# Performance work log

Hardware: AMD Instinct MI355X
Metric: run time of the kernel (lower is better)

The kernel has to match this reference:

```python
import jax, jax.numpy as jnp
import numpy as np

L = 4  # positional-encoding frequencies

def setup_inputs() -> dict:
    key = jax.random.key(0)
    ks = jax.random.split(key, 7)
    H, Wd, Ns = 512, 512, 8
    N = H * Wd * Ns
    f16 = jnp.float16
    return {
        "coords": jax.random.normal(ks[0], (N, 3), dtype=f16),
        "W1": (jax.random.normal(ks[1], (27, 64), dtype=jnp.float32) * 0.2).astype(f16),
        "b1": (jax.random.normal(ks[2], (64,), dtype=jnp.float32) * 0.02).astype(f16),
        "W2": (jax.random.normal(ks[3], (64, 64), dtype=jnp.float32) * 0.12).astype(f16),
        "b2": (jax.random.normal(ks[4], (64,), dtype=jnp.float32) * 0.02).astype(f16),
        "W3": (jax.random.normal(ks[5], (64, 4), dtype=jnp.float32) * 0.12).astype(f16),
        "b3": (jax.random.normal(ks[6], (4,), dtype=jnp.float32) * 0.02).astype(f16),
        "H": H,
        "W": Wd,
    }

def _positional_encoding(x):
    n = x.shape[0]
    freqs = (2.0 ** jnp.arange(L, dtype=jnp.float32)).astype(x.dtype)  # (L,)
    xf = x[:, None, :] * freqs[None, :, None]                          # (N, L, 3)
    sc = jnp.stack([jnp.sin(xf), jnp.cos(xf)], axis=2)                 # (N, L, 2, 3)
    return jnp.concatenate([x, sc.reshape(n, 2 * 3 * L)], axis=-1)

def _mlp(enc, W1, b1, W2, b2, W3, b3):
    h = jax.nn.relu(enc @ W1 + b1)
    h = jax.nn.relu(h @ W2 + b2)
    return h @ W3 + b3

def reference(coords, W1, b1, W2, b2, W3, b3, H, W):
    # The Python tile loop gathers idx_tile, runs PE+MLP, and scatters back to the
    # same idx_tile; the tiles partition [0, H*W*N_samples) exactly once, so the
    # whole forward equals a single fused PE+MLP over all coords.
    x = coords.astype(jnp.float16)
    enc = _positional_encoding(x)
    out = _mlp(enc, W1, b1, W2, b2, W3, b3)
    return out.astype(jnp.float16)  # (H*W*N_samples, 4)
```

## Files before the change

kernel.cpp:

```cpp
#include <hip/hip_runtime.h>

typedef _Float16 f16x2 __attribute__((ext_vector_type(2)));
typedef _Float16 f16x8 __attribute__((ext_vector_type(8)));
typedef float    floatx4 __attribute__((ext_vector_type(4)));
typedef unsigned uintx4 __attribute__((ext_vector_type(4)));

#define INV2PI 0.15915494309189535f
#define NP 4

__device__ __forceinline__ unsigned cvt_pk_u(float a, float b) {
    return __builtin_bit_cast(unsigned, __builtin_amdgcn_cvt_pkrtz(a, b));
}
__device__ __forceinline__ unsigned pk_relu_u(unsigned hu) {
    f16x2 h = __builtin_bit_cast(f16x2, hu);
    f16x2 z; z[0] = (_Float16)0.f; z[1] = (_Float16)0.f;
    return __builtin_bit_cast(unsigned, __builtin_elementwise_max(h, z));
}

__global__ __launch_bounds__(256, 4) void nerf_fused_kernel(
    const float* __restrict__ coords,
    const float* __restrict__ W1, const float* __restrict__ b1,
    const float* __restrict__ W2, const float* __restrict__ b2,
    const float* __restrict__ W3, const float* __restrict__ b3,
    float* __restrict__ out, int npts)
{
    __shared__ __align__(16) floatx4 wlds[14][64];

    const int tid  = threadIdx.x;
    const int wave = tid >> 6;
    const int lane = tid & 63;
    const int m    = lane & 15;
    const int g    = lane >> 4;

    if (wave == 0) {
        #pragma unroll
        for (int t1 = 0; t1 < 4; ++t1) {
            int n = t1 * 16 + m;
            f16x8 v;
            #pragma unroll
            for (int i = 0; i < 8; ++i) {
                float w;
                if (i < 6)        w = W1[(3 + 6 * g + (i >= 3 ? 3 : 0) + (i % 3)) * 64 + n];
                else if (g == 0)  w = (i == 6) ? W1[0 * 64 + n] : W1[1 * 64 + n];
                else if (g == 1)  w = (i == 6) ? W1[2 * 64 + n] : b1[n];
                else              w = 0.f;
                v[i] = (_Float16)w;
            }
            wlds[t1][lane] = __builtin_bit_cast(floatx4, v);
        }
        #pragma unroll
        for (int kk = 0; kk < 2; ++kk) {
            f16x8 v;
            #pragma unroll
            for (int i = 0; i < 8; ++i) {
                int f = ((i >> 2) + 2 * kk) * 16 + g * 4 + (i & 3);
                v[i] = (_Float16)((m < 4) ? W3[f * 4 + m] : 0.f);
            }
            wlds[12 + kk][lane] = __builtin_bit_cast(floatx4, v);
        }
    } else if (wave == 1) {
        #pragma unroll
        for (int t2 = 0; t2 < 4; ++t2) {
            int n = t2 * 16 + m;
            #pragma unroll
            for (int kk = 0; kk < 2; ++kk) {
                f16x8 v;
                #pragma unroll
                for (int i = 0; i < 8; ++i) {
                    int f = ((i >> 2) + 2 * kk) * 16 + g * 4 + (i & 3);
                    v[i] = (_Float16)W2[f * 64 + n];
                }
                wlds[4 + t2 * 2 + kk][lane] = __builtin_bit_cast(floatx4, v);
            }
        }
    }
    __syncthreads();

    floatx4 bias2q[4];
    #pragma unroll
    for (int t2 = 0; t2 < 4; ++t2)
        #pragma unroll
        for (int r = 0; r < 4; ++r)
            bias2q[t2][r] = b2[t2 * 16 + g * 4 + r];
    floatx4 bias3q;
    #pragma unroll
    for (int r = 0; r < 4; ++r)
        bias3q[r] = (g == 0) ? b3[r] : 0.f;
    const floatx4 zero4 = (floatx4){0.f, 0.f, 0.f, 0.f};

    const float sg = __builtin_amdgcn_ldexpf(INV2PI, g);

    const int  ntile = npts >> 6;
    const int  gw    = blockIdx.x * 4 + wave;
    const int  nw    = gridDim.x * 4;
    const int  niter = ntile / nw;

    const char* cptr = (const char*)coords + ((long)(gw << 6) + m) * 12;
    char*       optr = (char*)out + ((long)(gw << 6) + m) * 16;
    const long  cstride = (long)nw * 64 * 12;
    const long  ostride = (long)nw * 64 * 16;

    float cx[NP][3];
    #pragma unroll
    for (int p = 0; p < NP; ++p)
        #pragma unroll
        for (int j = 0; j < 3; ++j)
            cx[p][j] = *(const float*)(cptr + p * 192 + j * 4);
    cptr += cstride;

    for (int it = 0; it < niter; ++it) {
        unsigned fr0 = 0;
        asm volatile("" : "+v"(fr0));
        const floatx4* wp = &wlds[0][0] + fr0 + lane;

        f16x8 B1[NP];
        #pragma unroll
        for (int p = 0; p < NP; ++p) {
            float s[6];
            #pragma unroll
            for (int i = 0; i < 6; ++i) {
                float xv = cx[p][i % 3];
                float ph = (i >= 3) ? 0.25f : 0.f;
                s[i] = __builtin_amdgcn_sinf(fmaf(xv, sg, ph));
            }
            float v6 = (g == 0) ? cx[p][0] : ((g == 1) ? cx[p][2] : 0.f);
            float v7 = (g == 0) ? cx[p][1] : ((g == 1) ? 1.f : 0.f);
            uintx4 b1u;
            b1u[0] = cvt_pk_u(s[0], s[1]);
            b1u[1] = cvt_pk_u(s[2], s[3]);
            b1u[2] = cvt_pk_u(s[4], s[5]);
            b1u[3] = cvt_pk_u(v6, v7);
            B1[p] = __builtin_bit_cast(f16x8, b1u);
        }

        if (it + 1 < niter) {
            #pragma unroll
            for (int p = 0; p < NP; ++p)
                #pragma unroll
                for (int j = 0; j < 3; ++j)
                    cx[p][j] = *(const float*)(cptr + p * 192 + j * 4);
            cptr += cstride;
        }

        f16x8 B2[NP][2];
        #pragma unroll
        for (int kk = 0; kk < 2; ++kk) {
            uintx4 b2u[NP];
            #pragma unroll
            for (int tt = 0; tt < 2; ++tt) {
                f16x8 A1v = __builtin_bit_cast(f16x8, wp[(2 * kk + tt) * 64]);
                #pragma unroll
                for (int p = 0; p < NP; ++p) {
                    floatx4 a = __builtin_amdgcn_mfma_f32_16x16x32_f16(A1v, B1[p], zero4, 0, 0, 0);
                    b2u[p][2 * tt + 0] = pk_relu_u(cvt_pk_u(a[0], a[1]));
                    b2u[p][2 * tt + 1] = pk_relu_u(cvt_pk_u(a[2], a[3]));
                }
            }
            #pragma unroll
            for (int p = 0; p < NP; ++p)
                B2[p][kk] = __builtin_bit_cast(f16x8, b2u[p]);
        }

        f16x8 B3[NP][2];
        #pragma unroll
        for (int kk = 0; kk < 2; ++kk) {
            uintx4 b3u[NP];
            #pragma unroll
            for (int tt = 0; tt < 2; ++tt) {
                int t2 = 2 * kk + tt;
                f16x8 A2v0 = __builtin_bit_cast(f16x8, wp[(4 + t2 * 2) * 64]);
                f16x8 A2v1 = __builtin_bit_cast(f16x8, wp[(5 + t2 * 2) * 64]);
                #pragma unroll
                for (int p = 0; p < NP; ++p) {
                    floatx4 a = __builtin_amdgcn_mfma_f32_16x16x32_f16(A2v0, B2[p][0], bias2q[t2], 0, 0, 0);
                    a = __builtin_amdgcn_mfma_f32_16x16x32_f16(A2v1, B2[p][1], a, 0, 0, 0);
                    b3u[p][2 * tt + 0] = pk_relu_u(cvt_pk_u(a[0], a[1]));
                    b3u[p][2 * tt + 1] = pk_relu_u(cvt_pk_u(a[2], a[3]));
                }
            }
            #pragma unroll
            for (int p = 0; p < NP; ++p)
                B3[p][kk] = __builtin_bit_cast(f16x8, b3u[p]);
        }

        f16x8 A3v0 = __builtin_bit_cast(f16x8, wp[12 * 64]);
        f16x8 A3v1 = __builtin_bit_cast(f16x8, wp[13 * 64]);
        #pragma unroll
        for (int p = 0; p < NP; ++p) {
            floatx4 acc3 = __builtin_amdgcn_mfma_f32_16x16x32_f16(A3v0, B3[p][0], bias3q, 0, 0, 0);
            acc3 = __builtin_amdgcn_mfma_f32_16x16x32_f16(A3v1, B3[p][1], acc3, 0, 0, 0);
            if (g == 0)
                *(floatx4*)(optr + p * 256) = acc3;
        }
        optr += ostride;
    }
}

extern "C" void kernel_launch(void* const* d_in, const int* in_sizes, int n_in,
                              void* d_out, int out_size, void* d_ws, size_t ws_size,
                              hipStream_t stream) {
    const float* coords = (const float*)d_in[0];
    const float* W1 = (const float*)d_in[1];
    const float* b1 = (const float*)d_in[2];
    const float* W2 = (const float*)d_in[3];
    const float* b2 = (const float*)d_in[4];
    const float* W3 = (const float*)d_in[5];
    const float* b3 = (const float*)d_in[6];
    float* outp = (float*)d_out;

    const int npts = in_sizes[0] / 3;
    const int nblocks = 2048;
    hipLaunchKernelGGL(nerf_fused_kernel, dim3(nblocks), dim3(256), 0, stream,
                       coords, W1, b1, W2, b2, W3, b3, outp, npts);
}
```

Baseline: 39.27 us.

## Compute positional-encoding harmonics via double-angle recurrence and disable AGPR allocation

Result: slower. 41.71 us (+6.2%).

```diff
diff --git a/kernel.cpp b/kernel.cpp
--- a/kernel.cpp
+++ b/kernel.cpp
@@ -8,6 +8,15 @@
 #define INV2PI 0.15915494309189535f
 #define NP 4
 
+#if defined(__has_attribute)
+#if __has_attribute(amdgpu_agpr_alloc)
+#define NO_AGPR __attribute__((amdgpu_agpr_alloc(0)))
+#endif
+#endif
+#ifndef NO_AGPR
+#define NO_AGPR
+#endif
+
 __device__ __forceinline__ unsigned cvt_pk_u(float a, float b) {
     return __builtin_bit_cast(unsigned, __builtin_amdgcn_cvt_pkrtz(a, b));
 }
@@ -17,7 +26,7 @@
     return __builtin_bit_cast(unsigned, __builtin_elementwise_max(h, z));
 }
 
-__global__ __launch_bounds__(256, 4) void nerf_fused_kernel(
+__global__ __launch_bounds__(256, 4) NO_AGPR void nerf_fused_kernel(
     const float* __restrict__ coords,
     const float* __restrict__ W1, const float* __restrict__ b1,
     const float* __restrict__ W2, const float* __restrict__ b2,
@@ -40,10 +49,13 @@
             #pragma unroll
             for (int i = 0; i < 8; ++i) {
                 float w;
-                if (i < 6)        w = W1[(3 + 6 * g + (i >= 3 ? 3 : 0) + (i % 3)) * 64 + n];
-                else if (g == 0)  w = (i == 6) ? W1[0 * 64 + n] : W1[1 * 64 + n];
-                else if (g == 1)  w = (i == 6) ? W1[2 * 64 + n] : b1[n];
-                else              w = 0.f;
+                if (g < 3) {
+                    w = W1[(3 + 6 * (i >> 1) + 3 * (i & 1) + g) * 64 + n];
+                } else {
+                    if      (i < 3)  w = W1[i * 64 + n];
+                    else if (i == 3) w = b1[n];
+                    else             w = 0.f;
+                }
                 v[i] = (_Float16)w;
             }
             wlds[t1][lane] = __builtin_bit_cast(floatx4, v);
@@ -88,8 +100,6 @@
         bias3q[r] = (g == 0) ? b3[r] : 0.f;
     const floatx4 zero4 = (floatx4){0.f, 0.f, 0.f, 0.f};
 
-    const float sg = __builtin_amdgcn_ldexpf(INV2PI, g);
-
     const int  ntile = npts >> 6;
     const int  gw    = blockIdx.x * 4 + wave;
     const int  nw    = gridDim.x * 4;
@@ -116,20 +126,26 @@
         f16x8 B1[NP];
         #pragma unroll
         for (int p = 0; p < NP; ++p) {
-            float s[6];
-            #pragma unroll
-            for (int i = 0; i < 6; ++i) {
-                float xv = cx[p][i % 3];
-                float ph = (i >= 3) ? 0.25f : 0.f;
-                s[i] = __builtin_amdgcn_sinf(fmaf(xv, sg, ph));
-            }
-            float v6 = (g == 0) ? cx[p][0] : ((g == 1) ? cx[p][2] : 0.f);
-            float v7 = (g == 0) ? cx[p][1] : ((g == 1) ? 1.f : 0.f);
+            float xc = (g == 0) ? cx[p][0] : ((g == 1) ? cx[p][1] : cx[p][2]);
+            float th = xc * INV2PI;
+            float s  = __builtin_amdgcn_sinf(th);
+            float c  = __builtin_amdgcn_sinf(th + 0.25f);
             uintx4 b1u;
-            b1u[0] = cvt_pk_u(s[0], s[1]);
-            b1u[1] = cvt_pk_u(s[2], s[3]);
-            b1u[2] = cvt_pk_u(s[4], s[5]);
-            b1u[3] = cvt_pk_u(v6, v7);
+            b1u[0] = cvt_pk_u(s, c);
+            #pragma unroll
+            for (int l = 0; l < 3; ++l) {
+                float u  = s + s;
+                float cn = fmaf(-u, s, 1.f);
+                float sn = u * c;
+                s = sn; c = cn;
+                b1u[1 + l] = cvt_pk_u(s, c);
+            }
+            if (g == 3) {
+                b1u[0] = cvt_pk_u(cx[p][0], cx[p][1]);
+                b1u[1] = cvt_pk_u(cx[p][2], 1.f);
+                b1u[2] = 0u;
+                b1u[3] = 0u;
+            }
             B1[p] = __builtin_bit_cast(f16x8, b1u);
         }
 
```
